# Kernel optimization log

Measured on AMD Instinct MI355X. Metric: run time of the kernel, lower is better.

## Reference

```python
import jax, jax.numpy as jnp
import numpy as np

IN_NODES, OUT_NODES, F_SIZE = 4096, 1024, 16


def setup_inputs() -> dict:
    key = jax.random.key(0)
    u_hat = jax.random.normal(key, (IN_NODES * OUT_NODES, F_SIZE), dtype=jnp.float32)
    return {"u_hat": u_hat, "routing_num": 3}


def squash(s):
    # s: [out, f]
    sq = jnp.sum(s * s, axis=1, keepdims=True)
    return sq / (1.0 + sq) * (s / jnp.sqrt(sq))


def reference(u_hat, routing_num):
    # u_hat laid out edge-major as (in_node, out_node) blocks, matching DGL edge order
    uh = u_hat.reshape(IN_NODES, OUT_NODES, F_SIZE)
    b0 = jnp.zeros((IN_NODES, OUT_NODES), dtype=u_hat.dtype)

    def step(b, _):
        c = jax.nn.softmax(b, axis=1)                 # coupling coeffs over out capsules
        s = jnp.einsum('io,iof->of', c, uh)           # weighted message sum per out node
        v = squash(s)                                 # [out, f]
        b = b + jnp.einsum('iof,of->io', uh, v)       # agreement b-update
        return b, v

    _, vs = jax.lax.scan(step, b0, None, length=routing_num)
    return vs[-1]  # final out-capsule activations [OUT_NODES, F_SIZE]
```

## Files before the change

kernel.cpp:

```cpp
#include <hip/hip_runtime.h>
#include <math.h>

#define IN_NODES  4096
#define OUT_NODES 1024
#define ROW_ELEMS 16384
#define ROW_C4    4096
#define ROW_U4    2048
#define NG        256
#define PB        16

typedef unsigned short u16;
typedef unsigned int   u32;

__device__ __forceinline__ float dot4(const float4 a, const float4 b) {
    return a.x*b.x + a.y*b.y + a.z*b.z + a.w*b.w;
}
__device__ __forceinline__ void fma4(float4& a, const float c, const float4 u) {
    a.x += c*u.x; a.y += c*u.y; a.z += c*u.z; a.w += c*u.w;
}
__device__ __forceinline__ void add4(float4& a, const float4 u) {
    a.x += u.x; a.y += u.y; a.z += u.z; a.w += u.w;
}
__device__ __forceinline__ u16 f2b(float x) {
    u32 b = __float_as_uint(x);
    return (u16)((b + 0x7FFFu + ((b >> 16) & 1u)) >> 16);
}
__device__ __forceinline__ ushort4 f2b4(float4 v) {
    ushort4 r; r.x = f2b(v.x); r.y = f2b(v.y); r.z = f2b(v.z); r.w = f2b(v.w);
    return r;
}
__device__ __forceinline__ void unpack8(const uint4 w, float4& lo, float4& hi) {
    lo.x = __uint_as_float(w.x << 16);
    lo.y = __uint_as_float(w.x & 0xFFFF0000u);
    lo.z = __uint_as_float(w.y << 16);
    lo.w = __uint_as_float(w.y & 0xFFFF0000u);
    hi.x = __uint_as_float(w.z << 16);
    hi.y = __uint_as_float(w.z & 0xFFFF0000u);
    hi.z = __uint_as_float(w.w << 16);
    hi.w = __uint_as_float(w.w & 0xFFFF0000u);
}

__global__ __launch_bounds__(1024) void k_uniform(const float* __restrict__ uh,
                                                  u16* __restrict__ uh2,
                                                  float* __restrict__ part) {
    const int t    = threadIdx.x;
    const int wave = t >> 6;
    const int lane = t & 63;
    const int c0   = (wave << 8) + lane;

    float4 acc[4];
    #pragma unroll
    for (int j = 0; j < 4; ++j) acc[j] = make_float4(0.f, 0.f, 0.f, 0.f);

    const float4* p = reinterpret_cast<const float4*>(uh)
                    + (size_t)blockIdx.x * PB * ROW_C4 + c0;
    ushort4* q = reinterpret_cast<ushort4*>(uh2)
               + (size_t)blockIdx.x * PB * ROW_C4 + c0;

    for (int g = 0; g < PB; ++g) {
        float4 u[4];
        #pragma unroll
        for (int j = 0; j < 4; ++j) u[j] = p[j * 64];
        #pragma unroll
        for (int j = 0; j < 4; ++j) { add4(acc[j], u[j]); q[j * 64] = f2b4(u[j]); }
        p += ROW_C4; q += ROW_C4;
    }

    const float c = 1.0f / OUT_NODES;
    float4* sp = reinterpret_cast<float4*>(part) + (size_t)blockIdx.x * ROW_C4 + c0;
    #pragma unroll
    for (int j = 0; j < 4; ++j) {
        acc[j].x *= c; acc[j].y *= c; acc[j].z *= c; acc[j].w *= c;
        sp[j * 64] = acc[j];
    }
}

__global__ __launch_bounds__(1024) void k_soft(const u16* __restrict__ uh2,
                                               const float* __restrict__ V,
                                               float* __restrict__ part) {
    const int t    = threadIdx.x;
    const int wave = t >> 6;
    const int lane = t & 63;
    const int u0   = (wave << 7) + lane;

    __shared__ float2 red16[16];
    __shared__ float2 redS;

    float4 v[4];
    {
        const float4* vp = reinterpret_cast<const float4*>(V);
        v[0] = vp[2 * u0];          v[1] = vp[2 * u0 + 1];
        v[2] = vp[2 * (u0 + 64)];   v[3] = vp[2 * (u0 + 64) + 1];
    }

    float4 acc[4];
    #pragma unroll
    for (int j = 0; j < 4; ++j) acc[j] = make_float4(0.f, 0.f, 0.f, 0.f);

    const uint4* p = reinterpret_cast<const uint4*>(uh2)
                   + (size_t)blockIdx.x * PB * ROW_U4 + u0;

    uint4 cur[4];
    cur[0] = p[0]; cur[1] = p[64];
    cur[2] = p[ROW_U4]; cur[3] = p[ROW_U4 + 64];

    for (int g = 0; g < PB; g += 2) {
        uint4 nxt[4];
        const uint4* pn = p + 2 * ROW_U4;
        if (g + 2 < PB) {
            nxt[0] = pn[0]; nxt[1] = pn[64];
            nxt[2] = pn[ROW_U4]; nxt[3] = pn[ROW_U4 + 64];
        }

        float d[4];
        #pragma unroll
        for (int j = 0; j < 4; ++j) {
            float4 lo, hi;
            unpack8(cur[j], lo, hi);
            d[j] = dot4(lo, v[(j & 1) * 2]) + dot4(hi, v[(j & 1) * 2 + 1]);
        }
        #pragma unroll
        for (int j = 0; j < 4; ++j) d[j] += __shfl_xor(d[j], 1);

        float e[4];
        #pragma unroll
        for (int j = 0; j < 4; ++j) e[j] = __expf(d[j]);

        float ea = e[0] + e[1];
        float eb = e[2] + e[3];
        #pragma unroll
        for (int off = 32; off; off >>= 1) {
            ea += __shfl_xor(ea, off);
            eb += __shfl_xor(eb, off);
        }
        if (lane == 0) red16[wave] = make_float2(ea, eb);
        __syncthreads();
        if (wave == 0) {
            float2 s = (lane < 16) ? red16[lane] : make_float2(0.f, 0.f);
            #pragma unroll
            for (int off = 8; off; off >>= 1) {
                s.x += __shfl_xor(s.x, off);
                s.y += __shfl_xor(s.y, off);
            }
            if (lane == 0) redS = s;
        }
        __syncthreads();
        const float inva = 2.0f / redS.x;
        const float invb = 2.0f / redS.y;

        #pragma unroll
        for (int j = 0; j < 4; ++j) {
            float4 lo, hi;
            unpack8(cur[j], lo, hi);
            const float c = e[j] * ((j < 2) ? inva : invb);
            fma4(acc[(j & 1) * 2],     c, lo);
            fma4(acc[(j & 1) * 2 + 1], c, hi);
        }

        #pragma unroll
        for (int j = 0; j < 4; ++j) cur[j] = nxt[j];
        p = pn;
    }

    float4* sp = reinterpret_cast<float4*>(part) + (size_t)blockIdx.x * ROW_C4;
    sp[2 * u0]            = acc[0];
    sp[2 * u0 + 1]        = acc[1];
    sp[2 * (u0 + 64)]     = acc[2];
    sp[2 * (u0 + 64) + 1] = acc[3];
}

__global__ __launch_bounds__(256) void k_reduce(const float* __restrict__ part,
                                                float* __restrict__ V,
                                                float* __restrict__ out,
                                                int G, int first) {
    const int t    = threadIdx.x;
    const int gidx = blockIdx.x * 64 + (t >> 2);
    const int q    = t & 3;
    const float* p = part + gidx;
    float a0 = 0.f, a1 = 0.f;
    int b = q;
    for (; b + 4 < G; b += 8) {
        a0 += p[(size_t)(b    ) * ROW_ELEMS];
        a1 += p[(size_t)(b + 4) * ROW_ELEMS];
    }
    for (; b < G; b += 4) a0 += p[(size_t)b * ROW_ELEMS];
    float s = a0 + a1;
    s += __shfl_xor(s, 1);
    s += __shfl_xor(s, 2);

    float sq = s * s;
    sq += __shfl_xor(sq, 4);
    sq += __shfl_xor(sq, 8);
    sq += __shfl_xor(sq, 16);
    sq += __shfl_xor(sq, 32);

    const float scale = sq / ((1.0f + sq) * sqrtf(sq));
    const float v = s * scale;

    out[gidx] = v;
    V[gidx]   = first ? v : (V[gidx] + v);
}

__global__ __launch_bounds__(1024) void fb_uniform(const float* __restrict__ uh,
                                                   float* __restrict__ part,
                                                   int per_block) {
    const int t  = threadIdx.x;
    const int c0 = ((t >> 6) << 8) + (t & 63);
    float4 acc[4];
    #pragma unroll
    for (int j = 0; j < 4; ++j) acc[j] = make_float4(0.f, 0.f, 0.f, 0.f);
    const float4* p = reinterpret_cast<const float4*>(uh)
                    + (size_t)blockIdx.x * per_block * ROW_C4 + c0;
    for (int g = 0; g < per_block; ++g) {
        #pragma unroll
        for (int j = 0; j < 4; ++j) add4(acc[j], p[j * 64]);
        p += ROW_C4;
    }
    const float c = 1.0f / OUT_NODES;
    float4* sp = reinterpret_cast<float4*>(part) + (size_t)blockIdx.x * ROW_C4 + c0;
    #pragma unroll
    for (int j = 0; j < 4; ++j) {
        acc[j].x *= c; acc[j].y *= c; acc[j].z *= c; acc[j].w *= c;
        sp[j * 64] = acc[j];
    }
}

__global__ __launch_bounds__(1024) void fb_soft(const float* __restrict__ uh,
                                                const float* __restrict__ V,
                                                float* __restrict__ part,
                                                int per_block) {
    const int t    = threadIdx.x;
    const int wave = t >> 6;
    const int lane = t & 63;
    const int c0   = (wave << 8) + lane;
    __shared__ float red16[16];
    __shared__ float redS;

    float4 v[4];
    const float4* vp = reinterpret_cast<const float4*>(V) + c0;
    #pragma unroll
    for (int j = 0; j < 4; ++j) v[j] = vp[j * 64];

    float4 acc[4];
    #pragma unroll
    for (int j = 0; j < 4; ++j) acc[j] = make_float4(0.f, 0.f, 0.f, 0.f);

    const float4* p = reinterpret_cast<const float4*>(uh)
                    + (size_t)blockIdx.x * per_block * ROW_C4 + c0;
    for (int g = 0; g < per_block; ++g) {
        float4 u[4];
        #pragma unroll
        for (int j = 0; j < 4; ++j) u[j] = p[j * 64];
        float d[4];
        #pragma unroll
        for (int j = 0; j < 4; ++j) d[j] = dot4(u[j], v[j]);
        #pragma unroll
        for (int j = 0; j < 4; ++j) {
            d[j] += __shfl_xor(d[j], 1);
            d[j] += __shfl_xor(d[j], 2);
        }
        float e[4];
        float etot = 0.f;
        #pragma unroll
        for (int j = 0; j < 4; ++j) { e[j] = __expf(d[j]); etot += e[j]; }
        #pragma unroll
        for (int off = 32; off; off >>= 1) etot += __shfl_xor(etot, off);
        if (lane == 0) red16[wave] = etot;
        __syncthreads();
        if (wave == 0) {
            float s = (lane < 16) ? red16[lane] : 0.f;
            #pragma unroll
            for (int off = 8; off; off >>= 1) s += __shfl_xor(s, off);
            if (lane == 0) redS = s;
        }
        __syncthreads();
        const float inv = 4.0f / redS;
        #pragma unroll
        for (int j = 0; j < 4; ++j) fma4(acc[j], e[j] * inv, u[j]);
        p += ROW_C4;
    }
    float4* sp = reinterpret_cast<float4*>(part) + (size_t)blockIdx.x * ROW_C4 + c0;
    #pragma unroll
    for (int j = 0; j < 4; ++j) sp[j * 64] = acc[j];
}

extern "C" void kernel_launch(void* const* d_in, const int* in_sizes, int n_in,
                              void* d_out, int out_size, void* d_ws, size_t ws_size,
                              hipStream_t stream) {
    const float* uh  = (const float*)d_in[0];
    float*       out = (float*)d_out;

    char*  ws   = (char*)d_ws;
    float* V    = (float*)ws;
    float* part = (float*)(ws + 65536);
    u16*   uh2  = (u16*)(ws + 65536 + (size_t)NG * ROW_ELEMS * 4);

    const size_t need = 65536ull + (size_t)NG * ROW_ELEMS * 4ull
                      + (size_t)IN_NODES * ROW_ELEMS * 2ull;

    if (ws_size >= need) {
        k_uniform<<<NG, 1024, 0, stream>>>(uh, uh2, part);
        k_reduce<<<256, 256, 0, stream>>>(part, V, out, NG, 1);
        for (int it = 1; it < 3; ++it) {
            k_soft<<<NG, 1024, 0, stream>>>(uh2, V, part);
            k_reduce<<<256, 256, 0, stream>>>(part, V, out, NG, 0);
        }
    } else {
        int G2 = 256;
        while (G2 > 4 && ws_size < 65536ull * (size_t)(G2 + 1)) G2 >>= 1;
        const int per_block = IN_NODES / G2;
        fb_uniform<<<G2, 1024, 0, stream>>>(uh, part, per_block);
        k_reduce<<<256, 256, 0, stream>>>(part, V, out, G2, 1);
        for (int it = 1; it < 3; ++it) {
            fb_soft<<<G2, 1024, 0, stream>>>(uh, V, part, per_block);
            k_reduce<<<256, 256, 0, stream>>>(part, V, out, G2, 0);
        }
    }
}
```

Baseline: 162.0 us.

## Split soft-routing pass into 512 blocks of 512 threads, one row per step

The soft-routing kernel now launches 512 blocks of 512 threads instead of 256 blocks of 1024. Each iteration processes a single input row, with every thread handling four uint4 chunks, in place of two rows per iteration. The per-row softmax sum therefore needs one scalar reduction across 8 waves instead of a paired reduction across 16. The aim is higher occupancy and more blocks spread over the CUs. In exchange it doubles the partial-sum buffer and the work in the following reduce kernel, and raises register pressure with 8 accumulators and 8 cached V vectors per thread.

```diff
diff --git a/kernel.cpp b/kernel.cpp
--- a/kernel.cpp
+++ b/kernel.cpp
@@ -6,8 +6,8 @@
 #define ROW_ELEMS 16384
 #define ROW_C4    4096
 #define ROW_U4    2048
-#define NG        256
-#define PB        16
+#define G_UNI     256
+#define G_SOFT    512
 
 typedef unsigned short u16;
 typedef unsigned int   u32;
@@ -47,6 +47,7 @@
     const int wave = t >> 6;
     const int lane = t & 63;
     const int c0   = (wave << 8) + lane;
+    const int PB   = IN_NODES / G_UNI;
 
     float4 acc[4];
     #pragma unroll
@@ -75,41 +76,45 @@
     }
 }
 
-__global__ __launch_bounds__(1024) void k_soft(const u16* __restrict__ uh2,
-                                               const float* __restrict__ V,
-                                               float* __restrict__ part) {
+__global__ __launch_bounds__(512, 4) void k_soft(const u16* __restrict__ uh2,
+                                                 const float* __restrict__ V,
+                                                 float* __restrict__ part) {
     const int t    = threadIdx.x;
     const int wave = t >> 6;
     const int lane = t & 63;
-    const int u0   = (wave << 7) + lane;
-
-    __shared__ float2 red16[16];
-    __shared__ float2 redS;
-
-    float4 v[4];
+    const int PB   = IN_NODES / G_SOFT;
+
+    __shared__ float red8[8];
+    __shared__ float redS;
+
+    float4 v[8];
     {
         const float4* vp = reinterpret_cast<const float4*>(V);
-        v[0] = vp[2 * u0];          v[1] = vp[2 * u0 + 1];
-        v[2] = vp[2 * (u0 + 64)];   v[3] = vp[2 * (u0 + 64) + 1];
-    }
-
-    float4 acc[4];
-    #pragma unroll
-    for (int j = 0; j < 4; ++j) acc[j] = make_float4(0.f, 0.f, 0.f, 0.f);
+        #pragma unroll
+        for (int j = 0; j < 4; ++j) {
+            const int u = j * 512 + t;
+            v[2*j]   = vp[2*u];
+            v[2*j+1] = vp[2*u + 1];
+        }
+    }
+
+    float4 acc[8];
+    #pragma unroll
+    for (int j = 0; j < 8; ++j) acc[j] = make_float4(0.f, 0.f, 0.f, 0.f);
 
     const uint4* p = reinterpret_cast<const uint4*>(uh2)
-                   + (size_t)blockIdx.x * PB * ROW_U4 + u0;
+                   + (size_t)blockIdx.x * PB * ROW_U4;
 
     uint4 cur[4];
-    cur[0] = p[0]; cur[1] = p[64];
-    cur[2] = p[ROW_U4]; cur[3] = p[ROW_U4 + 64];
-
-    for (int g = 0; g < PB; g += 2) {
+    #pragma unroll
+    for (int j = 0; j < 4; ++j) cur[j] = p[j * 512 + t];
+
+    for (int g = 0; g < PB; ++g) {
         uint4 nxt[4];
-        const uint4* pn = p + 2 * ROW_U4;
-        if (g + 2 < PB) {
-            nxt[0] = pn[0]; nxt[1] = pn[64];
-            nxt[2] = pn[ROW_U4]; nxt[3] = pn[ROW_U4 + 64];
+        const uint4* pn = p + ROW_U4;
+        if (g + 1 < PB) {
+            #pragma unroll
+            for (int j = 0; j < 4; ++j) nxt[j] = pn[j * 512 + t];
         }
 
         float d[4];
@@ -117,7 +122,7 @@
         for (int j = 0; j < 4; ++j) {
             float4 lo, hi;
             unpack8(cur[j], lo, hi);
-            d[j] = dot4(lo, v[(j & 1) * 2]) + dot4(hi, v[(j & 1) * 2 + 1]);
+            d[j] = dot4(lo, v[2*j]) + dot4(hi, v[2*j+1]);
         }
         #pragma unroll
         for (int j = 0; j < 4; ++j) d[j] += __shfl_xor(d[j], 1);
@@ -126,35 +131,26 @@
         #pragma unroll
         for (int j = 0; j < 4; ++j) e[j] = __expf(d[j]);
 
-        float ea = e[0] + e[1];
-        float eb = e[2] + e[3];
-        #pragma unroll
-        for (int off = 32; off; off >>= 1) {
-            ea += __shfl_xor(ea, off);
-            eb += __shfl_xor(eb, off);
-        }
-        if (lane == 0) red16[wave] = make_float2(ea, eb);
+        float es = (e[0] + e[1]) + (e[2] + e[3]);
+        #pragma unroll
+        for (int off = 32; off; off >>= 1) es += __shfl_xor(es, off);
+        if (lane == 0) red8[wave] = es;
         __syncthreads();
         if (wave == 0) {
-            float2 s = (lane < 16) ? red16[lane] : make_float2(0.f, 0.f);
-            #pragma unroll
-            for (int off = 8; off; off >>= 1) {
-                s.x += __shfl_xor(s.x, off);
-                s.y += __shfl_xor(s.y, off);
-            }
+            float s = (lane < 8) ? red8[lane] : 0.f;
+            s += __shfl_xor(s, 4); s += __shfl_xor(s, 2); s += __shfl_xor(s, 1);
             if (lane == 0) redS = s;
         }
         __syncthreads();
-        const float inva = 2.0f / redS.x;
-        const float invb = 2.0f / redS.y;
+        const float inv = 2.0f / redS;
 
         #pragma unroll
         for (int j = 0; j < 4; ++j) {
             float4 lo, hi;
             unpack8(cur[j], lo, hi);
-            const float c = e[j] * ((j < 2) ? inva : invb);
-            fma4(acc[(j & 1) * 2],     c, lo);
-            fma4(acc[(j & 1) * 2 + 1], c, hi);
+            const float c = e[j] * inv;
+            fma4(acc[2*j],   c, lo);
+            fma4(acc[2*j+1], c, hi);
         }
 
         #pragma unroll
@@ -163,10 +159,12 @@
     }
 
     float4* sp = reinterpret_cast<float4*>(part) + (size_t)blockIdx.x * ROW_C4;
-    sp[2 * u0]            = acc[0];
-    sp[2 * u0 + 1]        = acc[1];
-    sp[2 * (u0 + 64)]     = acc[2];
-    sp[2 * (u0 + 64) + 1] = acc[3];
+    #pragma unroll
+    for (int j = 0; j < 4; ++j) {
+        const int u = j * 512 + t;
+        sp[2*u]     = acc[2*j];
+        sp[2*u + 1] = acc[2*j+1];
+    }
 }
 
 __global__ __launch_bounds__(256) void k_reduce(const float* __restrict__ part,
@@ -293,17 +291,17 @@
     char*  ws   = (char*)d_ws;
     float* V    = (float*)ws;
     float* part = (float*)(ws + 65536);
-    u16*   uh2  = (u16*)(ws + 65536 + (size_t)NG * ROW_ELEMS * 4);
-
-    const size_t need = 65536ull + (size_t)NG * ROW_ELEMS * 4ull
+    u16*   uh2  = (u16*)(ws + 65536 + (size_t)G_SOFT * ROW_ELEMS * 4);
+
+    const size_t need = 65536ull + (size_t)G_SOFT * ROW_ELEMS * 4ull
                       + (size_t)IN_NODES * ROW_ELEMS * 2ull;
 
     if (ws_size >= need) {
-        k_uniform<<<NG, 1024, 0, stream>>>(uh, uh2, part);
-        k_reduce<<<256, 256, 0, stream>>>(part, V, out, NG, 1);
+        k_uniform<<<G_UNI, 1024, 0, stream>>>(uh, uh2, part);
+        k_reduce<<<256, 256, 0, stream>>>(part, V, out, G_UNI, 1);
         for (int it = 1; it < 3; ++it) {
-            k_soft<<<NG, 1024, 0, stream>>>(uh2, V, part);
-            k_reduce<<<256, 256, 0, stream>>>(part, V, out, NG, 0);
+            k_soft<<<G_SOFT, 512, 0, stream>>>(uh2, V, part);
+            k_reduce<<<256, 256, 0, stream>>>(part, V, out, G_SOFT, 0);
         }
     } else {
         int G2 = 256;
```

Result: slower. 206.4 us (+27.4%).

## Split softmax kernel into denominator pass and accumulation pass to drop per-row barriers

Applied to the files above, without the earlier changes.

Rewrites the soft routing kernel as two phases. First, V is staged in shared memory and each wave computes the softmax denominator for one input row. Second, the whole block re-reads its rows, recomputes the dot products and accumulates the weighted sums, with no block-wide barriers inside the row loop. This removes the two __syncthreads per row pair, but the bf16 u_hat slice is read twice and 64KB of shared memory is used per block, which may limit occupancy.

```diff
diff --git a/kernel.cpp b/kernel.cpp
--- a/kernel.cpp
+++ b/kernel.cpp
@@ -75,98 +75,82 @@
     }
 }
 
-__global__ __launch_bounds__(1024) void k_soft(const u16* __restrict__ uh2,
-                                               const float* __restrict__ V,
-                                               float* __restrict__ part) {
+__global__ __launch_bounds__(1024) void k_soft2(const u16* __restrict__ uh2,
+                                                const float* __restrict__ V,
+                                                float* __restrict__ part) {
     const int t    = threadIdx.x;
     const int wave = t >> 6;
     const int lane = t & 63;
-    const int u0   = (wave << 7) + lane;
-
-    __shared__ float2 red16[16];
-    __shared__ float2 redS;
-
-    float4 v[4];
+
+    __shared__ float Vl[ROW_ELEMS];
+    __shared__ float invD[PB];
+
     {
         const float4* vp = reinterpret_cast<const float4*>(V);
-        v[0] = vp[2 * u0];          v[1] = vp[2 * u0 + 1];
-        v[2] = vp[2 * (u0 + 64)];   v[3] = vp[2 * (u0 + 64) + 1];
-    }
-
-    float4 acc[4];
-    #pragma unroll
-    for (int j = 0; j < 4; ++j) acc[j] = make_float4(0.f, 0.f, 0.f, 0.f);
-
-    const uint4* p = reinterpret_cast<const uint4*>(uh2)
-                   + (size_t)blockIdx.x * PB * ROW_U4 + u0;
-
-    uint4 cur[4];
-    cur[0] = p[0]; cur[1] = p[64];
-    cur[2] = p[ROW_U4]; cur[3] = p[ROW_U4 + 64];
-
-    for (int g = 0; g < PB; g += 2) {
-        uint4 nxt[4];
-        const uint4* pn = p + 2 * ROW_U4;
-        if (g + 2 < PB) {
-            nxt[0] = pn[0]; nxt[1] = pn[64];
-            nxt[2] = pn[ROW_U4]; nxt[3] = pn[ROW_U4 + 64];
-        }
-
-        float d[4];
-        #pragma unroll
-        for (int j = 0; j < 4; ++j) {
+        float4* vl = reinterpret_cast<float4*>(Vl);
+        #pragma unroll
+        for (int j = 0; j < 4; ++j) vl[j * 1024 + t] = vp[j * 1024 + t];
+    }
+    __syncthreads();
+
+    {
+        const uint4* row = reinterpret_cast<const uint4*>(uh2)
+                         + (size_t)(blockIdx.x * PB + wave) * ROW_U4;
+        float den = 0.f;
+        #pragma unroll 4
+        for (int k = 0; k < 32; ++k) {
+            const int u = k * 64 + lane;
+            const uint4 w = row[u];
+            const float4* vv = reinterpret_cast<const float4*>(Vl + u * 8);
             float4 lo, hi;
-            unpack8(cur[j], lo, hi);
-            d[j] = dot4(lo, v[(j & 1) * 2]) + dot4(hi, v[(j & 1) * 2 + 1]);
-        }
-        #pragma unroll
-        for (int j = 0; j < 4; ++j) d[j] += __shfl_xor(d[j], 1);
-
-        float e[4];
-        #pragma unroll
-        for (int j = 0; j < 4; ++j) e[j] = __expf(d[j]);
-
-        float ea = e[0] + e[1];
-        float eb = e[2] + e[3];
-        #pragma unroll
-        for (int off = 32; off; off >>= 1) {
-            ea += __shfl_xor(ea, off);
-            eb += __shfl_xor(eb, off);
-        }
-        if (lane == 0) red16[wave] = make_float2(ea, eb);
-        __syncthreads();
-        if (wave == 0) {
-            float2 s = (lane < 16) ? red16[lane] : make_float2(0.f, 0.f);
-            #pragma unroll
-            for (int off = 8; off; off >>= 1) {
-                s.x += __shfl_xor(s.x, off);
-                s.y += __shfl_xor(s.y, off);
-            }
-            if (lane == 0) redS = s;
-        }
-        __syncthreads();
-        const float inva = 2.0f / redS.x;
-        const float invb = 2.0f / redS.y;
-
-        #pragma unroll
-        for (int j = 0; j < 4; ++j) {
-            float4 lo, hi;
-            unpack8(cur[j], lo, hi);
-            const float c = e[j] * ((j < 2) ? inva : invb);
-            fma4(acc[(j & 1) * 2],     c, lo);
-            fma4(acc[(j & 1) * 2 + 1], c, hi);
-        }
-
-        #pragma unroll
-        for (int j = 0; j < 4; ++j) cur[j] = nxt[j];
-        p = pn;
+            unpack8(w, lo, hi);
+            float d = dot4(lo, vv[0]) + dot4(hi, vv[1]);
+            d += __shfl_xor(d, 1);
+            den += __expf(d);
+        }
+        #pragma unroll
+        for (int off = 32; off; off >>= 1) den += __shfl_xor(den, off);
+        if (lane == 0) invD[wave] = 2.0f / den;
+    }
+    __syncthreads();
+
+    float4 v0a = *reinterpret_cast<const float4*>(Vl + t * 8);
+    float4 v0b = *reinterpret_cast<const float4*>(Vl + t * 8 + 4);
+    float4 v1a = *reinterpret_cast<const float4*>(Vl + (t + 1024) * 8);
+    float4 v1b = *reinterpret_cast<const float4*>(Vl + (t + 1024) * 8 + 4);
+
+    float4 a0 = make_float4(0.f, 0.f, 0.f, 0.f), a1 = a0, a2 = a0, a3 = a0;
+
+    const uint4* base = reinterpret_cast<const uint4*>(uh2)
+                      + (size_t)blockIdx.x * PB * ROW_U4;
+    uint4 c0 = base[t], c1 = base[1024 + t];
+
+    for (int g = 0; g < PB; ++g) {
+        uint4 n0, n1;
+        const uint4* nb = base + (size_t)(g + 1) * ROW_U4;
+        if (g + 1 < PB) { n0 = nb[t]; n1 = nb[1024 + t]; }
+
+        const float iD = invD[g];
+        float4 lo0, hi0, lo1, hi1;
+        unpack8(c0, lo0, hi0);
+        unpack8(c1, lo1, hi1);
+        float d0 = dot4(lo0, v0a) + dot4(hi0, v0b);
+        float d1 = dot4(lo1, v1a) + dot4(hi1, v1b);
+        d0 += __shfl_xor(d0, 1);
+        d1 += __shfl_xor(d1, 1);
+        const float e0 = __expf(d0) * iD;
+        const float e1 = __expf(d1) * iD;
+        fma4(a0, e0, lo0); fma4(a1, e0, hi0);
+        fma4(a2, e1, lo1); fma4(a3, e1, hi1);
+
+        c0 = n0; c1 = n1;
     }
 
     float4* sp = reinterpret_cast<float4*>(part) + (size_t)blockIdx.x * ROW_C4;
-    sp[2 * u0]            = acc[0];
-    sp[2 * u0 + 1]        = acc[1];
-    sp[2 * (u0 + 64)]     = acc[2];
-    sp[2 * (u0 + 64) + 1] = acc[3];
+    sp[2 * t]              = a0;
+    sp[2 * t + 1]          = a1;
+    sp[2 * (1024 + t)]     = a2;
+    sp[2 * (1024 + t) + 1] = a3;
 }
 
 __global__ __launch_bounds__(256) void k_reduce(const float* __restrict__ part,
@@ -302,7 +286,7 @@
         k_uniform<<<NG, 1024, 0, stream>>>(uh, uh2, part);
         k_reduce<<<256, 256, 0, stream>>>(part, V, out, NG, 1);
         for (int it = 1; it < 3; ++it) {
-            k_soft<<<NG, 1024, 0, stream>>>(uh2, V, part);
+            k_soft2<<<NG, 1024, 0, stream>>>(uh2, V, part);
             k_reduce<<<256, 256, 0, stream>>>(part, V, out, NG, 0);
         }
     } else {
```

After: 337.4 us. 108% more time.

## Fuse all routing passes into one cooperative kernel with grid-wide syncs

Applied to the files above, without the earlier changes.

Replaces the chain of six kernel launches (uniform pass, reductions, two softmax passes) with one cooperative kernel that uses grid.sync() between phases. The per-capsule reduction and squash are folded in, with each block reducing 64 output elements across all partials. This is meant to remove launch gaps and per-kernel ramp-up, at the cost of grid barriers and a cooperative launch of 256 blocks of 1024 threads. The small-workspace fallback path is dropped, so when the workspace is too small nothing is computed.

```diff
diff --git a/kernel.cpp b/kernel.cpp
--- a/kernel.cpp
+++ b/kernel.cpp
@@ -1,5 +1,8 @@
 #include <hip/hip_runtime.h>
+#include <hip/hip_cooperative_groups.h>
 #include <math.h>
+
+namespace cg = cooperative_groups;
 
 #define IN_NODES  4096
 #define OUT_NODES 1024
@@ -40,6 +43,167 @@
     hi.w = __uint_as_float(w.w & 0xFFFF0000u);
 }
 
+__global__ __launch_bounds__(1024)
+void fused_route(const float* __restrict__ uh, u16* __restrict__ uh2,
+                 float* __restrict__ part, float* __restrict__ V,
+                 float* __restrict__ out) {
+    cg::grid_group grid = cg::this_grid();
+    const int t    = threadIdx.x;
+    const int wave = t >> 6;
+    const int lane = t & 63;
+    const int blk  = blockIdx.x;
+
+    __shared__ float2 red16[16];
+    __shared__ float2 redS;
+    __shared__ float  sred[16][64];
+
+    {
+        const int c0 = (wave << 8) + lane;
+        float4 acc[4];
+        #pragma unroll
+        for (int j = 0; j < 4; ++j) acc[j] = make_float4(0.f, 0.f, 0.f, 0.f);
+
+        const float4* p = reinterpret_cast<const float4*>(uh)
+                        + (size_t)blk * PB * ROW_C4 + c0;
+        ushort4* q = reinterpret_cast<ushort4*>(uh2)
+                   + (size_t)blk * PB * ROW_C4 + c0;
+
+        for (int g = 0; g < PB; ++g) {
+            float4 u[4];
+            #pragma unroll
+            for (int j = 0; j < 4; ++j) u[j] = p[j * 64];
+            #pragma unroll
+            for (int j = 0; j < 4; ++j) { add4(acc[j], u[j]); q[j * 64] = f2b4(u[j]); }
+            p += ROW_C4; q += ROW_C4;
+        }
+
+        const float c = 1.0f / OUT_NODES;
+        float4* sp = reinterpret_cast<float4*>(part) + (size_t)blk * ROW_C4 + c0;
+        #pragma unroll
+        for (int j = 0; j < 4; ++j) {
+            acc[j].x *= c; acc[j].y *= c; acc[j].z *= c; acc[j].w *= c;
+            sp[j * 64] = acc[j];
+        }
+    }
+    grid.sync();
+
+    for (int it = 0; it < 3; ++it) {
+        {
+            const float* pp = part + blk * 64 + lane;
+            float s0 = 0.f, s1 = 0.f;
+            for (int b = wave; b < NG; b += 32) {
+                s0 += pp[(size_t)b * ROW_ELEMS];
+                s1 += pp[(size_t)(b + 16) * ROW_ELEMS];
+            }
+            sred[wave][lane] = s0 + s1;
+            __syncthreads();
+            if (wave == 0) {
+                float s = 0.f;
+                #pragma unroll
+                for (int w = 0; w < 16; ++w) s += sred[w][lane];
+                float sq = s * s;
+                sq += __shfl_xor(sq, 1);
+                sq += __shfl_xor(sq, 2);
+                sq += __shfl_xor(sq, 4);
+                sq += __shfl_xor(sq, 8);
+                const float scale = sq / ((1.0f + sq) * sqrtf(sq));
+                const float v = s * scale;
+                const int g = blk * 64 + lane;
+                V[g] = (it == 0) ? v : (V[g] + v);
+                if (it == 2) out[g] = v;
+            }
+        }
+        if (it == 2) break;
+        grid.sync();
+
+        {
+            const int u0 = (wave << 7) + lane;
+            float4 v[4];
+            {
+                const float4* vp = reinterpret_cast<const float4*>(V);
+                v[0] = vp[2 * u0];          v[1] = vp[2 * u0 + 1];
+                v[2] = vp[2 * (u0 + 64)];   v[3] = vp[2 * (u0 + 64) + 1];
+            }
+
+            float4 acc[4];
+            #pragma unroll
+            for (int j = 0; j < 4; ++j) acc[j] = make_float4(0.f, 0.f, 0.f, 0.f);
+
+            const uint4* p = reinterpret_cast<const uint4*>(uh2)
+                           + (size_t)blk * PB * ROW_U4 + u0;
+
+            uint4 cur[4];
+            cur[0] = p[0];      cur[1] = p[64];
+            cur[2] = p[ROW_U4]; cur[3] = p[ROW_U4 + 64];
+
+            for (int g = 0; g < PB; g += 2) {
+                uint4 nxt[4];
+                const uint4* pn = p + 2 * ROW_U4;
+                if (g + 2 < PB) {
+                    nxt[0] = pn[0];      nxt[1] = pn[64];
+                    nxt[2] = pn[ROW_U4]; nxt[3] = pn[ROW_U4 + 64];
+                }
+
+                float d[4];
+                #pragma unroll
+                for (int j = 0; j < 4; ++j) {
+                    float4 lo, hi;
+                    unpack8(cur[j], lo, hi);
+                    d[j] = dot4(lo, v[(j & 1) * 2]) + dot4(hi, v[(j & 1) * 2 + 1]);
+                }
+                #pragma unroll
+                for (int j = 0; j < 4; ++j) d[j] += __shfl_xor(d[j], 1);
+
+                float e[4];
+                #pragma unroll
+                for (int j = 0; j < 4; ++j) e[j] = __expf(d[j]);
+
+                float ea = e[0] + e[1];
+                float eb = e[2] + e[3];
+                #pragma unroll
+                for (int off = 32; off; off >>= 1) {
+                    ea += __shfl_xor(ea, off);
+                    eb += __shfl_xor(eb, off);
+                }
+                if (lane == 0) red16[wave] = make_float2(ea, eb);
+                __syncthreads();
+                if (wave == 0) {
+                    float2 qv = (lane < 16) ? red16[lane] : make_float2(0.f, 0.f);
+                    #pragma unroll
+                    for (int off = 8; off; off >>= 1) {
+                        qv.x += __shfl_xor(qv.x, off);
+                        qv.y += __shfl_xor(qv.y, off);
+                    }
+                    if (lane == 0) redS = qv;
+                }
+                __syncthreads();
+                const float inva = 2.0f / redS.x;
+                const float invb = 2.0f / redS.y;
+
+                #pragma unroll
+                for (int j = 0; j < 4; ++j) {
+                    float4 lo, hi;
+                    unpack8(cur[j], lo, hi);
+                    const float c = e[j] * ((j < 2) ? inva : invb);
+                    fma4(acc[(j & 1) * 2],     c, lo);
+                    fma4(acc[(j & 1) * 2 + 1], c, hi);
+                }
+
+                #pragma unroll
+                for (int j = 0; j < 4; ++j) cur[j] = nxt[j];
+                p = pn;
+            }
+
+            float4* sp = reinterpret_cast<float4*>(part) + (size_t)blk * ROW_C4;
+            sp[2 * u0]            = acc[0];
+            sp[2 * u0 + 1]        = acc[1];
+            sp[2 * (u0 + 64)]     = acc[2];
+            sp[2 * (u0 + 64) + 1] = acc[3];
+        }
+        grid.sync();
+    }
+}
+
 __global__ __launch_bounds__(1024) void k_uniform(const float* __restrict__ uh,
                                                   u16* __restrict__ uh2,
                                                   float* __restrict__ part) {
@@ -101,14 +265,14 @@
                    + (size_t)blockIdx.x * PB * ROW_U4 + u0;
 
     uint4 cur[4];
-    cur[0] = p[0]; cur[1] = p[64];
+    cur[0] = p[0];      cur[1] = p[64];
     cur[2] = p[ROW_U4]; cur[3] = p[ROW_U4 + 64];
 
     for (int g = 0; g < PB; g += 2) {
         uint4 nxt[4];
         const uint4* pn = p + 2 * ROW_U4;
         if (g + 2 < PB) {
-            nxt[0] = pn[0]; nxt[1] = pn[64];
+            nxt[0] = pn[0];      nxt[1] = pn[64];
             nxt[2] = pn[ROW_U4]; nxt[3] = pn[ROW_U4 + 64];
         }
 
@@ -136,13 +300,13 @@
         if (lane == 0) red16[wave] = make_float2(ea, eb);
         __syncthreads();
         if (wave == 0) {
-            float2 s = (lane < 16) ? red16[lane] : make_float2(0.f, 0.f);
+            float2 qv = (lane < 16) ? red16[lane] : make_float2(0.f, 0.f);
             #pragma unroll
             for (int off = 8; off; off >>= 1) {
-                s.x += __shfl_xor(s.x, off);
-                s.y += __shfl_xor(s.y, off);
+                qv.x += __shfl_xor(qv.x, off);
+                qv.y += __shfl_xor(qv.y, off);
             }
-            if (lane == 0) redS = s;
+            if (lane == 0) redS = qv;
         }
         __syncthreads();
         const float inva = 2.0f / redS.x;
@@ -201,89 +365,6 @@
     V[gidx]   = first ? v : (V[gidx] + v);
 }
 
-__global__ __launch_bounds__(1024) void fb_uniform(const float* __restrict__ uh,
-                                                   float* __restrict__ part,
-                                                   int per_block) {
-    const int t  = threadIdx.x;
-    const int c0 = ((t >> 6) << 8) + (t & 63);
-    float4 acc[4];
-    #pragma unroll
-    for (int j = 0; j < 4; ++j) acc[j] = make_float4(0.f, 0.f, 0.f, 0.f);
-    const float4* p = reinterpret_cast<const float4*>(uh)
-                    + (size_t)blockIdx.x * per_block * ROW_C4 + c0;
-    for (int g = 0; g < per_block; ++g) {
-        #pragma unroll
-        for (int j = 0; j < 4; ++j) add4(acc[j], p[j * 64]);
-        p += ROW_C4;
-    }
-    const float c = 1.0f / OUT_NODES;
-    float4* sp = reinterpret_cast<float4*>(part) + (size_t)blockIdx.x * ROW_C4 + c0;
-    #pragma unroll
-    for (int j = 0; j < 4; ++j) {
-        acc[j].x *= c; acc[j].y *= c; acc[j].z *= c; acc[j].w *= c;
-        sp[j * 64] = acc[j];
-    }
-}
-
-__global__ __launch_bounds__(1024) void fb_soft(const float* __restrict__ uh,
-                                                const float* __restrict__ V,
-                                                float* __restrict__ part,
-                                                int per_block) {
-    const int t    = threadIdx.x;
-    const int wave = t >> 6;
-    const int lane = t & 63;
-    const int c0   = (wave << 8) + lane;
-    __shared__ float red16[16];
-    __shared__ float redS;
-
-    float4 v[4];
-    const float4* vp = reinterpret_cast<const float4*>(V) + c0;
-    #pragma unroll
-    for (int j = 0; j < 4; ++j) v[j] = vp[j * 64];
-
-    float4 acc[4];
-    #pragma unroll
-    for (int j = 0; j < 4; ++j) acc[j] = make_float4(0.f, 0.f, 0.f, 0.f);
-
-    const float4* p = reinterpret_cast<const float4*>(uh)
-                    + (size_t)blockIdx.x * per_block * ROW_C4 + c0;
-    for (int g = 0; g < per_block; ++g) {
-        float4 u[4];
-        #pragma unroll
-        for (int j = 0; j < 4; ++j) u[j] = p[j * 64];
-        float d[4];
-        #pragma unroll
-        for (int j = 0; j < 4; ++j) d[j] = dot4(u[j], v[j]);
-        #pragma unroll
-        for (int j = 0; j < 4; ++j) {
-            d[j] += __shfl_xor(d[j], 1);
-            d[j] += __shfl_xor(d[j], 2);
-        }
-        float e[4];
-        float etot = 0.f;
-        #pragma unroll
-        for (int j = 0; j < 4; ++j) { e[j] = __expf(d[j]); etot += e[j]; }
-        #pragma unroll
-        for (int off = 32; off; off >>= 1) etot += __shfl_xor(etot, off);
-        if (lane == 0) red16[wave] = etot;
-        __syncthreads();
-        if (wave == 0) {
-            float s = (lane < 16) ? red16[lane] : 0.f;
-            #pragma unroll
-            for (int off = 8; off; off >>= 1) s += __shfl_xor(s, off);
-            if (lane == 0) redS = s;
-        }
-        __syncthreads();
-        const float inv = 4.0f / redS;
-        #pragma unroll
-        for (int j = 0; j < 4; ++j) fma4(acc[j], e[j] * inv, u[j]);
-        p += ROW_C4;
-    }
-    float4* sp = reinterpret_cast<float4*>(part) + (size_t)blockIdx.x * ROW_C4 + c0;
-    #pragma unroll
-    for (int j = 0; j < 4; ++j) sp[j * 64] = acc[j];
-}
-
 extern "C" void kernel_launch(void* const* d_in, const int* in_sizes, int n_in,
                               void* d_out, int out_size, void* d_ws, size_t ws_size,
                               hipStream_t stream) {
@@ -298,22 +379,22 @@
     const size_t need = 65536ull + (size_t)NG * ROW_ELEMS * 4ull
                       + (size_t)IN_NODES * ROW_ELEMS * 2ull;
 
+    bool ok = false;
     if (ws_size >= need) {
+        void* args[] = { (void*)&uh, (void*)&uh2, (void*)&part,
+                         (void*)&V, (void*)&out };
+        hipError_t e = hipLaunchCooperativeKernel((const void*)fused_route,
+                                                  dim3(NG), dim3(1024),
+                                                  args, 0, stream);
+        ok = (e == hipSuccess);
+    }
+
+    if (!ok && ws_size >= need) {
         k_uniform<<<NG, 1024, 0, stream>>>(uh, uh2, part);
         k_reduce<<<256, 256, 0, stream>>>(part, V, out, NG, 1);
         for (int it = 1; it < 3; ++it) {
             k_soft<<<NG, 1024, 0, stream>>>(uh2, V, part);
             k_reduce<<<256, 256, 0, stream>>>(part, V, out, NG, 0);
         }
-    } else {
-        int G2 = 256;
-        while (G2 > 4 && ws_size < 65536ull * (size_t)(G2 + 1)) G2 >>= 1;
-        const int per_block = IN_NODES / G2;
-        fb_uniform<<<G2, 1024, 0, stream>>>(uh, part, per_block);
-        k_reduce<<<256, 256, 0, stream>>>(part, V, out, G2, 1);
-        for (int it = 1; it < 3; ++it) {
-            fb_soft<<<G2, 1024, 0, stream>>>(uh, V, part, per_block);
-            k_reduce<<<256, 256, 0, stream>>>(part, V, out, G2, 0);
-        }
-    }
-}
+    }
+}
```

New measurement: 309.6 us. 1.91x slower.
